# Optimization experiments

Measured on AMD Instinct MI355X. Metric: run time of the kernel, lower is better.

The kernel has to match this reference:

```python
import jax, jax.numpy as jnp
import numpy as np

HRNN = 2e-11  # seconds per step; t grid is in nanoseconds (x1e9), step = 0.02
W0, W1 = -20.0, 10.0          # fixed oscillator coupling weights
X0 = (0.4736, 0.8745, 1.8497)  # fixed initial state


def setup_inputs() -> dict:
    key = jax.random.key(0)
    ks = jax.random.split(key, 9)
    B, T, NIN, NHI, NHO, NOUT = 1024, 2048, 8, 64, 64, 1
    g = lambda k, shape, s: jax.random.normal(k, shape, jnp.float32) * s
    return {
        "inputdata": jax.random.normal(ks[0], (B, T, NIN), jnp.float32),
        "Wni": g(ks[1], (NHI, NIN), 1.0 / np.sqrt(NIN)),   # nonlinearinput
        "bni": g(ks[2], (NHI,), 0.1),
        "Wli": g(ks[3], (1, NHI), 1.0 / np.sqrt(NHI)),     # linearinput
        "bli": g(ks[4], (1,), 0.1),
        "tau": jnp.zeros((1,), jnp.float32),                # nn.Parameter(Tensor(1))
        "Wn": g(ks[5], (NHO, 3), 1.0 / np.sqrt(3.0)),      # nonlinear readout
        "bn": g(ks[6], (NHO,), 0.1),
        "Wl": g(ks[7], (NOUT, NHO), 1.0 / np.sqrt(NHO)),   # linear readout
        "bl": g(ks[8], (NOUT,), 0.1),
    }


def reference(inputdata, Wni, bni, Wli, bli, tau, Wn, bn, Wl, bl):
    B, T, NIN = inputdata.shape
    tg = jnp.linspace(0.0, HRNN * (T - 1) * 1e9, T).astype(jnp.float32)
    u = inputdata  # [B, T, NIN]
    x0 = jnp.broadcast_to(jnp.array(X0, jnp.float32)[None, :], (B, 3))

    def lin_interp(t):
        # clamp-to-edge linear interpolation of u along the time grid
        ind = jnp.clip(jnp.searchsorted(tg, t), 1, T - 1)
        t_lo, t_hi = tg[ind - 1], tg[ind]
        frac = jnp.clip((t - t_lo) / (t_hi - t_lo), 0.0, 1.0)
        u_lo = u[:, ind - 1, :]
        return u_lo + (u[:, ind, :] - u_lo) * frac  # [B, NIN]

    def f(t, x):
        ut = lin_interp(t)
        dparam = jax.nn.sigmoid(ut @ Wni.T + bni) @ Wli.T + bli  # [B, 1]
        tx = jnp.tanh(x)
        dx = jnp.stack(
            (-x[:, 0] + tx[:, 1],
             -x[:, 1] + tx[:, 2],
             -x[:, 2] + W0 * tx[:, 0] + W1 * tx[:, 1]),
            axis=1,
        )
        return dx / jnp.exp(tau + dparam)  # [B, 3]

    def step(x, ts):
        # torchdiffeq 'rk4' = fourth-order 3/8 rule between grid points
        t0, t1 = ts
        h = t1 - t0
        k1 = f(t0, x)
        k2 = f(t0 + h / 3, x + h * k1 / 3)
        k3 = f(t0 + 2 * h / 3, x + h * (k2 - k1 / 3))
        k4 = f(t1, x + h * (k1 - k2 + k3))
        xn = x + h * (k1 + 3 * k2 + 3 * k3 + k4) / 8
        return xn, xn

    _, xs = jax.lax.scan(step, x0, (tg[:-1], tg[1:]))  # [T-1, B, 3]
    outrnn = jnp.concatenate([x0[None], xs], axis=0).transpose(1, 0, 2)  # [B, T, 3]
    hid = jax.nn.sigmoid(outrnn @ Wn.T + bn)  # [B, T, NHO]
    return hid @ Wl.T + bl  # [B, T, NOUT]
```

## Files before the change

### kernel.cpp

```cpp
#include <hip/hip_runtime.h>

#define BB 1024
#define TT 2048
#define NIN 8
#define NHI 64

#define CS 2.8853900817779268f
#define ICS (1.0f / CS)
#define NL2E 1.4426950408889634f
#define DELTA (40.94f / 2047.0f)

__device__ __forceinline__ float sig_pre(float zs) {
    float e = __builtin_amdgcn_exp2f(zs);
    return __builtin_amdgcn_rcpf(1.0f + e);
}

template<int CTRL>
__device__ __forceinline__ float qperm(float x) {
    int r = __builtin_amdgcn_mov_dpp(__float_as_int(x), CTRL, 0xF, 0xF, true);
    return __int_as_float(r);
}

__global__ __launch_bounds__(256) void precompute_r(
    const float* __restrict__ u, const float* __restrict__ Wni,
    const float* __restrict__ bni, const float* __restrict__ Wli,
    const float* __restrict__ bli, const float* __restrict__ tau,
    float* __restrict__ r3)
{
    __shared__ float sWni[NHI * NIN];
    __shared__ float sbni[NHI];
    __shared__ float sWli[NHI];
    int lt = threadIdx.x;
    for (int i = lt; i < NHI * NIN; i += 256) sWni[i] = Wni[i] * -NL2E;
    if (lt < NHI) { sbni[lt] = bni[lt] * -NL2E; sWli[lt] = Wli[lt]; }
    __syncthreads();

    int lane = lt & 63;
    long long gw = (long long)blockIdx.x * 4 + (lt >> 6);
    int b = (int)(gw / 33);
    int chunk = (int)(gw % 33);
    int s = chunk * 63 + lane;
    int sc = s < TT ? s : TT - 1;

    const float4* up4 = reinterpret_cast<const float4*>(u + ((long long)b * TT + sc) * NIN);
    float4 uA = up4[0], uB = up4[1];

    float d0 = 0.f, d1 = 0.f, d2 = 0.f;
    #pragma unroll 8
    for (int j = 0; j < NHI; j++) {
        const float* wj = &sWni[j * NIN];
        float z = sbni[j];
        z = fmaf(wj[0], uA.x, z); z = fmaf(wj[1], uA.y, z);
        z = fmaf(wj[2], uA.z, z); z = fmaf(wj[3], uA.w, z);
        z = fmaf(wj[4], uB.x, z); z = fmaf(wj[5], uB.y, z);
        z = fmaf(wj[6], uB.z, z); z = fmaf(wj[7], uB.w, z);
        float zn = __shfl_down(z, 1);
        float dz = zn - z;
        float z1 = fmaf(dz, 1.0f / 3.0f, z);
        float z2 = fmaf(dz, 2.0f / 3.0f, z);
        float wl = sWli[j];
        d0 = fmaf(wl, sig_pre(z),  d0);
        d1 = fmaf(wl, sig_pre(z1), d1);
        d2 = fmaf(wl, sig_pre(z2), d2);
    }
    float base = tau[0] + bli[0];
    float r0 = __builtin_amdgcn_exp2f((base + d0) * -NL2E);
    float r1 = __builtin_amdgcn_exp2f((base + d1) * -NL2E);
    float r2 = __builtin_amdgcn_exp2f((base + d2) * -NL2E);

    if (s < TT) {
        float* p = r3 + ((long long)b * TT + s) * 3;
        p[0] = r0;
        if (lane < 63 && s < TT - 1) { p[1] = r1; p[2] = r2; }
    }
}

__global__ __launch_bounds__(64) void scan_kernel(
    const float* __restrict__ r3, float* __restrict__ xs)
{
    int gt = blockIdx.x * 64 + threadIdx.x;
    int b = gt >> 2;
    int l = gt & 3;

    const float4* rp = reinterpret_cast<const float4*>(r3 + (long long)b * TT * 3);
    int comp = (l == 3) ? 1 : l;
    float* xc = xs + (long long)comp * BB * TT + (long long)b * TT;

    const float h = DELTA;
    bool is2 = (l == 2);
    float cA = is2 ? 40.0f * CS : -2.0f * CS;
    float cB = is2 ? -20.0f * CS : 0.0f;
    float Kl = is2 ? -10.0f * CS : CS;

    float X = (l == 0) ? 0.4736f * CS : (is2 ? 1.8497f * CS : 0.8745f * CS);

#define STEP(R1v, R2v, R3v, R4v) do { \
    float g1 = h * (R1v), g2 = h * (R2v), g3 = h * (R3v); \
    float q  = g1 * (1.0f / 3.0f); \
    float g4_8 = (h * (R4v)) * 0.125f; \
    float cA1 = q * cA,    cB1 = q * cB; \
    float cA2 = g2 * cA,   cB2 = g2 * cB; \
    float cA3 = g3 * cA,   cB3 = g3 * cB; \
    float cA4 = g4_8 * cA, cB4 = g4_8 * cB; \
     \
    float e1 = __builtin_amdgcn_exp2f(X); \
    float rho1 = __builtin_amdgcn_rcpf(1.0f + e1); \
    float KmX = Kl - X; \
    float pb2 = fmaf(q, KmX, X); \
    float p11 = qperm<0x89>(rho1), p21 = qperm<0x10>(rho1); \
    float S2 = fmaf(cA1, p11, fmaf(cB1, p21, pb2)); \
    float V1 = fmaf(cA, p11, cB * p21); \
    float W1 = V1 + KmX; \
     \
    float e2 = __builtin_amdgcn_exp2f(S2); \
    float rho2 = __builtin_amdgcn_rcpf(1.0f + e2); \
    float KmS2 = Kl - S2; \
    float pb3 = fmaf(g2, KmS2, fmaf(-q, W1, X)); \
    float p12 = qperm<0x89>(rho2), p22 = qperm<0x10>(rho2); \
    float S3 = fmaf(cA2, p12, fmaf(cB2, p22, pb3)); \
    float V2 = fmaf(cA, p12, cB * p22); \
    float W2 = V2 + KmS2; \
     \
    float e3 = __builtin_amdgcn_exp2f(S3); \
    float rho3 = __builtin_amdgcn_rcpf(1.0f + e3); \
    float KmS3 = Kl - S3; \
    float pb4 = fmaf(g3, KmS3, fmaf(-g2, W2, fmaf(g1, W1, X))); \
    float p13 = qperm<0x89>(rho3), p23 = qperm<0x10>(rho3); \
    float S4 = fmaf(cA3, p13, fmaf(cB3, p23, pb4)); \
    float V3 = fmaf(cA, p13, cB * p23); \
    float W3 = V3 + KmS3; \
     \
    float e4 = __builtin_amdgcn_exp2f(S4); \
    float rho4 = __builtin_amdgcn_rcpf(1.0f + e4); \
    float KmS4 = Kl - S4; \
    float t3 = fmaf(3.0f * g3, W3, fmaf(3.0f * g2, W2, g1 * W1)); \
    float pbX = fmaf(g4_8, KmS4, fmaf(0.125f, t3, X)); \
    float p14 = qperm<0x89>(rho4), p24 = qperm<0x10>(rho4); \
    X = fmaf(cA4, p14, fmaf(cB4, p24, pbX)); \
} while (0)

    float4 f0 = rp[0], f1 = rp[1], f2 = rp[2];
    float4 n0 = rp[3], n1 = rp[4], n2 = rp[5];

    for (int j = 0; j < 510; j++) {
        float4 m0 = rp[3 * j + 6], m1 = rp[3 * j + 7], m2 = rp[3 * j + 8];
        float4 ov;
        ov.x = X * ICS;
        STEP(f0.x, f0.y, f0.z, f0.w);  ov.y = X * ICS;
        STEP(f0.w, f1.x, f1.y, f1.z);  ov.z = X * ICS;
        STEP(f1.z, f1.w, f2.x, f2.y);  ov.w = X * ICS;
        *reinterpret_cast<float4*>(xc + 4 * j) = ov;
        STEP(f2.y, f2.z, f2.w, n0.x);
        f0 = n0; f1 = n1; f2 = n2;
        n0 = m0; n1 = m1; n2 = m2;
    }
    {
        float4 ov;
        ov.x = X * ICS;
        STEP(f0.x, f0.y, f0.z, f0.w);  ov.y = X * ICS;
        STEP(f0.w, f1.x, f1.y, f1.z);  ov.z = X * ICS;
        STEP(f1.z, f1.w, f2.x, f2.y);  ov.w = X * ICS;
        *reinterpret_cast<float4*>(xc + 4 * 510) = ov;
        STEP(f2.y, f2.z, f2.w, n0.x);
        f0 = n0; f1 = n1; f2 = n2;
    }
    {
        float4 ov;
        ov.x = X * ICS;
        STEP(f0.x, f0.y, f0.z, f0.w);  ov.y = X * ICS;
        STEP(f0.w, f1.x, f1.y, f1.z);  ov.z = X * ICS;
        STEP(f1.z, f1.w, f2.x, f2.y);  ov.w = X * ICS;
        *reinterpret_cast<float4*>(xc + 4 * 511) = ov;
    }
#undef STEP
}

__global__ __launch_bounds__(256) void out_kernel(
    const float* __restrict__ xs, const float* __restrict__ Wn,
    const float* __restrict__ bn, const float* __restrict__ Wl,
    const float* __restrict__ bl, float* __restrict__ out)
{
    __shared__ float sWn[NHI * 3];
    __shared__ float sbn[NHI];
    __shared__ float sWl[NHI];
    int lt = threadIdx.x;
    if (lt < NHI * 3) sWn[lt] = Wn[lt] * -NL2E;
    if (lt < NHI) { sbn[lt] = bn[lt] * -NL2E; sWl[lt] = Wl[lt]; }
    __syncthreads();

    long long tid = (long long)blockIdx.x * 256 + lt;
    float c0 = xs[tid];
    float c1 = xs[(long long)BB * TT + tid];
    float c2 = xs[(long long)2 * BB * TT + tid];
    float acc = 0.0f;
    #pragma unroll 8
    for (int j = 0; j < NHI; j++) {
        float z = fmaf(sWn[j * 3], c0,
                  fmaf(sWn[j * 3 + 1], c1,
                  fmaf(sWn[j * 3 + 2], c2, sbn[j])));
        acc = fmaf(sWl[j], sig_pre(z), acc);
    }
    out[tid] = acc + bl[0];
}

extern "C" void kernel_launch(void* const* d_in, const int* in_sizes, int n_in,
                              void* d_out, int out_size, void* d_ws, size_t ws_size,
                              hipStream_t stream) {
    const float* u    = (const float*)d_in[0];
    const float* Wni  = (const float*)d_in[1];
    const float* bni  = (const float*)d_in[2];
    const float* Wli  = (const float*)d_in[3];
    const float* bli  = (const float*)d_in[4];
    const float* tau  = (const float*)d_in[5];
    const float* Wn   = (const float*)d_in[6];
    const float* bn   = (const float*)d_in[7];
    const float* Wl   = (const float*)d_in[8];
    const float* bl   = (const float*)d_in[9];
    float* out = (float*)d_out;

    float* r3 = (float*)d_ws;
    float* xs = r3 + (size_t)3 * BB * TT;

    precompute_r<<<(BB * 33) / 4, 256, 0, stream>>>(u, Wni, bni, Wli, bli, tau, r3);
    scan_kernel<<<(BB * 4) / 64, 64, 0, stream>>>(r3, xs);
    out_kernel<<<(BB * TT) / 256, 256, 0, stream>>>(xs, Wn, bn, Wl, bl, out);
}
```

Baseline: 437.9 us.

## Read weights directly, factor sigmoid exps, fold step into coefficients, enlarge scan blocks

In precompute, the three sigmoid exponentials per hidden unit become two: exp(z) and exp(dz/3), with the midpoint values obtained by multiplication. The step size DELTA is now folded into the stored coefficients, so the scan no longer multiplies by h. Both precompute and output kernels drop their LDS staging and barrier and read the weights directly from global memory as uniform loads. The scan kernel moves from 64-thread to 512-thread blocks, which packs the serial scan onto far fewer CUs and may lengthen its latency-bound critical path.

```diff
diff --git a/kernel.cpp b/kernel.cpp
--- a/kernel.cpp
+++ b/kernel.cpp
@@ -27,14 +27,7 @@
     const float* __restrict__ bli, const float* __restrict__ tau,
     float* __restrict__ r3)
 {
-    __shared__ float sWni[NHI * NIN];
-    __shared__ float sbni[NHI];
-    __shared__ float sWli[NHI];
     int lt = threadIdx.x;
-    for (int i = lt; i < NHI * NIN; i += 256) sWni[i] = Wni[i] * -NL2E;
-    if (lt < NHI) { sbni[lt] = bni[lt] * -NL2E; sWli[lt] = Wli[lt]; }
-    __syncthreads();
-
     int lane = lt & 63;
     long long gw = (long long)blockIdx.x * 4 + (lt >> 6);
     int b = (int)(gw / 33);
@@ -48,37 +41,39 @@
     float d0 = 0.f, d1 = 0.f, d2 = 0.f;
     #pragma unroll 8
     for (int j = 0; j < NHI; j++) {
-        const float* wj = &sWni[j * NIN];
-        float z = sbni[j];
+        const float* wj = Wni + j * NIN;
+        float z = bni[j];
         z = fmaf(wj[0], uA.x, z); z = fmaf(wj[1], uA.y, z);
         z = fmaf(wj[2], uA.z, z); z = fmaf(wj[3], uA.w, z);
         z = fmaf(wj[4], uB.x, z); z = fmaf(wj[5], uB.y, z);
         z = fmaf(wj[6], uB.z, z); z = fmaf(wj[7], uB.w, z);
         float zn = __shfl_down(z, 1);
         float dz = zn - z;
-        float z1 = fmaf(dz, 1.0f / 3.0f, z);
-        float z2 = fmaf(dz, 2.0f / 3.0f, z);
-        float wl = sWli[j];
-        d0 = fmaf(wl, sig_pre(z),  d0);
-        d1 = fmaf(wl, sig_pre(z1), d1);
-        d2 = fmaf(wl, sig_pre(z2), d2);
+        float e0  = __builtin_amdgcn_exp2f(z * -NL2E);
+        float edz = __builtin_amdgcn_exp2f(dz * (-NL2E / 3.0f));
+        float e1 = e0 * edz;
+        float e2 = e1 * edz;
+        float wl = Wli[j];
+        d0 = fmaf(wl, __builtin_amdgcn_rcpf(1.0f + e0), d0);
+        d1 = fmaf(wl, __builtin_amdgcn_rcpf(1.0f + e1), d1);
+        d2 = fmaf(wl, __builtin_amdgcn_rcpf(1.0f + e2), d2);
     }
     float base = tau[0] + bli[0];
-    float r0 = __builtin_amdgcn_exp2f((base + d0) * -NL2E);
-    float r1 = __builtin_amdgcn_exp2f((base + d1) * -NL2E);
-    float r2 = __builtin_amdgcn_exp2f((base + d2) * -NL2E);
+    float g0 = DELTA * __builtin_amdgcn_exp2f((base + d0) * -NL2E);
+    float g1 = DELTA * __builtin_amdgcn_exp2f((base + d1) * -NL2E);
+    float g2 = DELTA * __builtin_amdgcn_exp2f((base + d2) * -NL2E);
 
     if (s < TT) {
         float* p = r3 + ((long long)b * TT + s) * 3;
-        p[0] = r0;
-        if (lane < 63 && s < TT - 1) { p[1] = r1; p[2] = r2; }
-    }
-}
-
-__global__ __launch_bounds__(64) void scan_kernel(
+        p[0] = g0;
+        if (lane < 63 && s < TT - 1) { p[1] = g1; p[2] = g2; }
+    }
+}
+
+__global__ __launch_bounds__(512) void scan_kernel(
     const float* __restrict__ r3, float* __restrict__ xs)
 {
-    int gt = blockIdx.x * 64 + threadIdx.x;
+    int gt = blockIdx.x * 512 + threadIdx.x;
     int b = gt >> 2;
     int l = gt & 3;
 
@@ -86,7 +81,6 @@
     int comp = (l == 3) ? 1 : l;
     float* xc = xs + (long long)comp * BB * TT + (long long)b * TT;
 
-    const float h = DELTA;
     bool is2 = (l == 2);
     float cA = is2 ? 40.0f * CS : -2.0f * CS;
     float cB = is2 ? -20.0f * CS : 0.0f;
@@ -94,10 +88,10 @@
 
     float X = (l == 0) ? 0.4736f * CS : (is2 ? 1.8497f * CS : 0.8745f * CS);
 
-#define STEP(R1v, R2v, R3v, R4v) do { \
-    float g1 = h * (R1v), g2 = h * (R2v), g3 = h * (R3v); \
+#define STEP(G1v, G2v, G3v, G4v) do { \
+    float g1 = (G1v), g2 = (G2v), g3 = (G3v); \
     float q  = g1 * (1.0f / 3.0f); \
-    float g4_8 = (h * (R4v)) * 0.125f; \
+    float g4_8 = (G4v) * 0.125f; \
     float cA1 = q * cA,    cB1 = q * cB; \
     float cA2 = g2 * cA,   cB2 = g2 * cB; \
     float cA3 = g3 * cA,   cB3 = g3 * cB; \
@@ -180,25 +174,19 @@
     const float* __restrict__ bn, const float* __restrict__ Wl,
     const float* __restrict__ bl, float* __restrict__ out)
 {
-    __shared__ float sWn[NHI * 3];
-    __shared__ float sbn[NHI];
-    __shared__ float sWl[NHI];
     int lt = threadIdx.x;
-    if (lt < NHI * 3) sWn[lt] = Wn[lt] * -NL2E;
-    if (lt < NHI) { sbn[lt] = bn[lt] * -NL2E; sWl[lt] = Wl[lt]; }
-    __syncthreads();
-
     long long tid = (long long)blockIdx.x * 256 + lt;
     float c0 = xs[tid];
     float c1 = xs[(long long)BB * TT + tid];
     float c2 = xs[(long long)2 * BB * TT + tid];
+    float cs0 = c0 * -NL2E, cs1 = c1 * -NL2E, cs2 = c2 * -NL2E;
     float acc = 0.0f;
     #pragma unroll 8
     for (int j = 0; j < NHI; j++) {
-        float z = fmaf(sWn[j * 3], c0,
-                  fmaf(sWn[j * 3 + 1], c1,
-                  fmaf(sWn[j * 3 + 2], c2, sbn[j])));
-        acc = fmaf(sWl[j], sig_pre(z), acc);
+        float zs = fmaf(Wn[j * 3], cs0,
+                   fmaf(Wn[j * 3 + 1], cs1,
+                   fmaf(Wn[j * 3 + 2], cs2, bn[j] * -NL2E)));
+        acc = fmaf(Wl[j], sig_pre(zs), acc);
     }
     out[tid] = acc + bl[0];
 }
@@ -222,6 +210,6 @@
     float* xs = r3 + (size_t)3 * BB * TT;
 
     precompute_r<<<(BB * 33) / 4, 256, 0, stream>>>(u, Wni, bni, Wli, bli, tau, r3);
-    scan_kernel<<<(BB * 4) / 64, 64, 0, stream>>>(r3, xs);
+    scan_kernel<<<(BB * 4) / 512, 512, 0, stream>>>(r3, xs);
     out_kernel<<<(BB * TT) / 256, 256, 0, stream>>>(xs, Wn, bn, Wl, bl, out);
 }
```

After: 677.3 us. 54.7% more time.
